# Kernel optimization log

Hardware: AMD Instinct MI355X
Metric: run time of the kernel (lower is better)

The kernel has to match this reference:

```python
import jax, jax.numpy as jnp
import numpy as np

DIM = 1024
H = 16
HD = 64

def setup_inputs() -> dict:
    key = jax.random.key(0)
    ks = jax.random.split(key, 5)
    x = jax.random.normal(ks[0], (2, 2048, DIM), dtype=jnp.float32)
    gamma = jnp.ones((DIM,), jnp.float32)
    beta = jnp.zeros((DIM,), jnp.float32)
    w_qkv = jax.random.normal(ks[1], (DIM, 3 * H * HD), dtype=jnp.float32) * (DIM ** -0.5)
    w_out = jax.random.normal(ks[2], (H * HD, DIM), dtype=jnp.float32) * ((H * HD) ** -0.5)
    b_out = jnp.zeros((DIM,), jnp.float32)
    return {"x": x, "gamma": gamma, "beta": beta, "w_qkv": w_qkv, "w_out": w_out, "b_out": b_out}

def reference(x, gamma, beta, w_qkv, w_out, b_out):
    # LayerNorm (pre-norm)
    mu = jnp.mean(x, axis=-1, keepdims=True)
    var = jnp.var(x, axis=-1, keepdims=True)
    xn = (x - mu) * jax.lax.rsqrt(var + 1e-5) * gamma + beta
    # QKV projection (no bias)
    qkv = xn @ w_qkv  # (b, n, 3*h*hd)
    q, k, v = jnp.split(qkv, 3, axis=-1)
    b, n, _ = x.shape
    split = lambda t: t.reshape(b, n, H, HD).transpose(0, 2, 1, 3)  # b h n d
    q, k, v = split(q), split(k), split(v)
    scale = HD ** -0.5
    scores = jnp.einsum('bhqd,bhkd->bhqk', q, k) * scale
    weights = jax.nn.softmax(scores, axis=-1)
    attn = jnp.einsum('bhqk,bhkd->bhqd', weights, v)  # b h n d
    attn = attn.transpose(0, 2, 1, 3).reshape(b, n, H * HD)
    # output projection (dropout is identity in eval)
    return attn @ w_out + b_out
```

## Files before the change

### kernel.cpp

```cpp
#include <hip/hip_runtime.h>
#include <hip/hip_bf16.h>


typedef _Float16 f16x8 __attribute__((ext_vector_type(8)));
typedef _Float16 f16x4 __attribute__((ext_vector_type(4)));
typedef float    f32x4 __attribute__((ext_vector_type(4)));

#define DIM   1024
#define NH    16
#define HD2   64
#define SEQ   2048
#define ROWS  4096
#define QKVN  3072

__device__ __forceinline__ void async_copy16(void* lds, const void* gsrc) {
    __builtin_amdgcn_global_load_lds(
        (const __attribute__((address_space(1))) unsigned int*)gsrc,
        (__attribute__((address_space(3))) unsigned int*)lds, 16, 0, 0);
}

__global__ __launch_bounds__(256) void prologue_kernel(
    const float* __restrict__ x, const float* __restrict__ gamma,
    const float* __restrict__ beta, _Float16* __restrict__ xn,
    const float* __restrict__ w_qkv, _Float16* __restrict__ wqkvT,
    const float* __restrict__ w_out, _Float16* __restrict__ woutT) {
    __shared__ float smem[32 * 33];
    const int bid = blockIdx.x;
    const int t = threadIdx.x;
    if (bid < ROWS) {
        const int row = bid;
        const float4 v = reinterpret_cast<const float4*>(x + (size_t)row * DIM)[t];
        float s1 = v.x + v.y + v.z + v.w;
        float s2 = v.x * v.x + v.y * v.y + v.z * v.z + v.w * v.w;
        for (int off = 32; off; off >>= 1) {
            s1 += __shfl_down(s1, off);
            s2 += __shfl_down(s2, off);
        }
        const int wv = t >> 6, lane = t & 63;
        if (lane == 0) { smem[wv * 2] = s1; smem[wv * 2 + 1] = s2; }
        __syncthreads();
        s1 = smem[0] + smem[2] + smem[4] + smem[6];
        s2 = smem[1] + smem[3] + smem[5] + smem[7];
        const float mu = s1 * (1.0f / DIM);
        const float var = s2 * (1.0f / DIM) - mu * mu;
        const float rstd = rsqrtf(var + 1e-5f);
        const float4 g = reinterpret_cast<const float4*>(gamma)[t];
        const float4 bb = reinterpret_cast<const float4*>(beta)[t];
        f16x4 o;
        o[0] = (_Float16)((v.x - mu) * rstd * g.x + bb.x);
        o[1] = (_Float16)((v.y - mu) * rstd * g.y + bb.y);
        o[2] = (_Float16)((v.z - mu) * rstd * g.z + bb.z);
        o[3] = (_Float16)((v.w - mu) * rstd * g.w + bb.w);
        reinterpret_cast<f16x4*>(xn + (size_t)row * DIM)[t] = o;
        return;
    }
    const float* in;
    _Float16* out;
    int C, bx, by;
    if (bid < ROWS + (QKVN / 32) * (DIM / 32)) {
        const int q = bid - ROWS;
        in = w_qkv; out = wqkvT; C = QKVN;
        bx = q % (QKVN / 32); by = q / (QKVN / 32);
    } else {
        const int q = bid - ROWS - (QKVN / 32) * (DIM / 32);
        in = w_out; out = woutT; C = DIM;
        bx = q % (DIM / 32); by = q / (DIM / 32);
    }
    const int R = DIM;
    const int c0 = bx * 32, r0 = by * 32;
    const int tx = t & 31, ty = t >> 5;
    float (*tile)[33] = reinterpret_cast<float(*)[33]>(smem);
#pragma unroll
    for (int i = 0; i < 4; i++)
        tile[ty + i * 8][tx] = in[(size_t)(r0 + ty + i * 8) * C + c0 + tx];
    __syncthreads();
#pragma unroll
    for (int i = 0; i < 4; i++)
        out[(size_t)(c0 + ty + i * 8) * R + r0 + tx] = (_Float16)tile[tx][ty + i * 8];
}

__global__ __launch_bounds__(256) void gemm_qkv_kernel(
    const _Float16* __restrict__ A, const _Float16* __restrict__ Bt,
    _Float16* __restrict__ qk, _Float16* __restrict__ vT, int K) {
    __shared__ _Float16 Al[2][128 * 32];
    __shared__ _Float16 Bl[2][128 * 32];
    const int t = threadIdx.x, wv = t >> 6, lane = t & 63;
    const int lg = lane >> 4, lr = lane & 15;
    const int wr = wv >> 1, wc = wv & 1;
    const int id = blockIdx.x;
    const int nid = (id & 7) * 96 + (id >> 3);
    const int bx = nid / 32, by = nid % 32;
    const int m0 = by * 128, n0 = bx * 128;

    f32x4 acc[4][4] = {};

    const int srow = t >> 2, sk = (t & 3) * 8;
    const _Float16* Ag0 = A + (size_t)(m0 + srow) * K + sk;
    const _Float16* Bg0 = Bt + (size_t)(n0 + srow) * K + sk;

    auto STAGE = [&](int buf, int k0) {
        _Float16* Alw = &Al[buf][wv * 512];
        _Float16* Blw = &Bl[buf][wv * 512];
        async_copy16(Alw,        Ag0 + k0);
        async_copy16(Alw + 2048, Ag0 + (size_t)64 * K + k0);
        async_copy16(Blw,        Bg0 + k0);
        async_copy16(Blw + 2048, Bg0 + (size_t)64 * K + k0);
    };

    STAGE(0, 0);
    asm volatile("s_waitcnt vmcnt(0)" ::: "memory");
    __builtin_amdgcn_s_barrier();
    int cur = 0;
    for (int k0 = 0; k0 < K; k0 += 32) {
        if (k0 + 32 < K) STAGE(cur ^ 1, k0 + 32);
        const _Float16* Ab = &Al[cur][0];
        const _Float16* Bb = &Bl[cur][0];
        f16x8 af[4], bfr[4];
#pragma unroll
        for (int m = 0; m < 4; m++)
            af[m] = *reinterpret_cast<const f16x8*>(&Ab[(wr * 64 + m * 16 + lr) * 32 + lg * 8]);
#pragma unroll
        for (int n = 0; n < 4; n++)
            bfr[n] = *reinterpret_cast<const f16x8*>(&Bb[(wc * 64 + n * 16 + lr) * 32 + lg * 8]);
#pragma unroll
        for (int m = 0; m < 4; m++)
#pragma unroll
            for (int n = 0; n < 4; n++)
                acc[m][n] = __builtin_amdgcn_mfma_f32_16x16x32_f16(af[m], bfr[n], acc[m][n], 0, 0, 0);
        asm volatile("s_waitcnt vmcnt(0)" ::: "memory");
        __builtin_amdgcn_s_barrier();
        cur ^= 1;
    }

    if (n0 < 2 * DIM) {
#pragma unroll
        for (int m = 0; m < 4; m++) {
            const int row = m0 + wr * 64 + m * 16 + lg * 4;
#pragma unroll
            for (int n = 0; n < 4; n++) {
                const int col = n0 + wc * 64 + n * 16 + lr;
#pragma unroll
                for (int jj = 0; jj < 4; jj++)
                    qk[(size_t)(row + jj) * 2048 + col] = (_Float16)acc[m][n][jj];
            }
        }
    } else {
#pragma unroll
        for (int m = 0; m < 4; m++) {
            const int row = m0 + wr * 64 + m * 16 + lg * 4;
            const int b = row >> 11, nn = row & 2047;
#pragma unroll
            for (int n = 0; n < 4; n++) {
                const int vcol = n0 + wc * 64 + n * 16 + lr - 2 * DIM;
                f16x4 pk;
#pragma unroll
                for (int jj = 0; jj < 4; jj++) pk[jj] = (_Float16)acc[m][n][jj];
                *reinterpret_cast<f16x4*>(&vT[(size_t)(b * 1024 + vcol) * SEQ + nn]) = pk;
            }
        }
    }
}

__global__ __launch_bounds__(256) void gemm_out_kernel(
    const _Float16* __restrict__ A, const _Float16* __restrict__ Bt,
    float* __restrict__ C, const float* __restrict__ bias, int N, int K) {
    __shared__ _Float16 Al[2][128 * 32];
    __shared__ _Float16 Bl[2][64 * 32];
    const int t = threadIdx.x, wv = t >> 6, lane = t & 63;
    const int lg = lane >> 4, lr = lane & 15;
    const int wr = wv >> 1, wc = wv & 1;
    const int id = blockIdx.x;
    const int nid = (id & 7) * 64 + (id >> 3);
    const int bx = nid / 32, by = nid % 32;
    const int m0 = by * 128, n0 = bx * 64;

    f32x4 acc[4][2] = {};

    const int srow = t >> 2, sk = (t & 3) * 8;
    const _Float16* Ag0 = A + (size_t)(m0 + srow) * K + sk;
    const _Float16* Bg0 = Bt + (size_t)(n0 + srow) * K + sk;

    auto STAGE = [&](int buf, int k0) {
        _Float16* Alw = &Al[buf][wv * 512];
        _Float16* Blw = &Bl[buf][wv * 512];
        async_copy16(Alw,        Ag0 + k0);
        async_copy16(Alw + 2048, Ag0 + (size_t)64 * K + k0);
        async_copy16(Blw,        Bg0 + k0);
    };

    STAGE(0, 0);
    asm volatile("s_waitcnt vmcnt(0)" ::: "memory");
    __builtin_amdgcn_s_barrier();
    int cur = 0;
    for (int k0 = 0; k0 < K; k0 += 32) {
        if (k0 + 32 < K) STAGE(cur ^ 1, k0 + 32);
        const _Float16* Ab = &Al[cur][0];
        const _Float16* Bb = &Bl[cur][0];
        f16x8 af[4], bfr[2];
#pragma unroll
        for (int m = 0; m < 4; m++)
            af[m] = *reinterpret_cast<const f16x8*>(&Ab[(wr * 64 + m * 16 + lr) * 32 + lg * 8]);
#pragma unroll
        for (int n = 0; n < 2; n++)
            bfr[n] = *reinterpret_cast<const f16x8*>(&Bb[(wc * 32 + n * 16 + lr) * 32 + lg * 8]);
#pragma unroll
        for (int m = 0; m < 4; m++)
#pragma unroll
            for (int n = 0; n < 2; n++)
                acc[m][n] = __builtin_amdgcn_mfma_f32_16x16x32_f16(af[m], bfr[n], acc[m][n], 0, 0, 0);
        asm volatile("s_waitcnt vmcnt(0)" ::: "memory");
        __builtin_amdgcn_s_barrier();
        cur ^= 1;
    }

#pragma unroll
    for (int m = 0; m < 4; m++) {
        const int row = m0 + wr * 64 + m * 16 + lg * 4;
#pragma unroll
        for (int n = 0; n < 2; n++) {
            const int col = n0 + wc * 32 + n * 16 + lr;
            const float bo = bias[col];
#pragma unroll
            for (int jj = 0; jj < 4; jj++)
                C[(size_t)(row + jj) * N + col] = acc[m][n][jj] + bo;
        }
    }
}

__global__ __launch_bounds__(256, 2) void attn_fa_kernel(
    const _Float16* __restrict__ qk, const _Float16* __restrict__ vT,
    _Float16* __restrict__ attn) {
    const int id = blockIdx.x;
    const int nid = (id & 7) * 64 + (id >> 3);
    const int bh = nid >> 4, b = bh >> 4, h = bh & 15;
    const int q0 = (nid & 15) * 128;
    const int t = threadIdx.x, wv = t >> 6, lane = t & 63;
    const int lg = lane >> 4, lr = lane & 15;

    __shared__ _Float16 Kl[2][64][76];
    __shared__ _Float16 Vt[2][64][76];

    const _Float16* qb = qk + (size_t)(b * SEQ + q0 + wv * 32 + lr) * 2048 + h * HD2;
    f16x8 qf[2][2];
    qf[0][0] = *reinterpret_cast<const f16x8*>(qb + lg * 8);
    qf[0][1] = *reinterpret_cast<const f16x8*>(qb + 32 + lg * 8);
    qf[1][0] = *reinterpret_cast<const f16x8*>(qb + (size_t)16 * 2048 + lg * 8);
    qf[1][1] = *reinterpret_cast<const f16x8*>(qb + (size_t)16 * 2048 + 32 + lg * 8);
#pragma unroll
    for (int qs = 0; qs < 2; qs++) {
        qf[qs][0] = qf[qs][0] * (_Float16)0.125f;
        qf[qs][1] = qf[qs][1] * (_Float16)0.125f;
    }

    f32x4 o[2][4] = {};
    float mrun[2] = {-INFINITY, -INFINITY}, lrun[2] = {0.f, 0.f};

    const int sr = t >> 3, sc = (t & 7) * 8;
    const _Float16* kbase = qk + (size_t)(b * SEQ + sr) * 2048 + DIM + h * HD2 + sc;
    const _Float16* vbase = vT + (size_t)(bh * HD2 + sr) * SEQ + sc;

    f16x8 rk0 = *reinterpret_cast<const f16x8*>(kbase);
    f16x8 rk1 = *reinterpret_cast<const f16x8*>(kbase + (size_t)32 * 2048);
    f16x8 rv0 = *reinterpret_cast<const f16x8*>(vbase);
    f16x8 rv1 = *reinterpret_cast<const f16x8*>(vbase + (size_t)32 * SEQ);
    *reinterpret_cast<f16x8*>(&Kl[0][sr][sc])      = rk0;
    *reinterpret_cast<f16x8*>(&Kl[0][sr + 32][sc]) = rk1;
    *reinterpret_cast<f16x8*>(&Vt[0][sr][sc])      = rv0;
    *reinterpret_cast<f16x8*>(&Vt[0][sr + 32][sc]) = rv1;
    rk0 = *reinterpret_cast<const f16x8*>(kbase + (size_t)64 * 2048);
    rk1 = *reinterpret_cast<const f16x8*>(kbase + (size_t)96 * 2048);
    rv0 = *reinterpret_cast<const f16x8*>(vbase + 64);
    rv1 = *reinterpret_cast<const f16x8*>(vbase + (size_t)32 * SEQ + 64);
    asm volatile("s_waitcnt lgkmcnt(0)" ::: "memory");
    __builtin_amdgcn_s_barrier();

    int p = 0;
    for (int kv0 = 0; kv0 < SEQ; kv0 += 64, p ^= 1) {
        if (kv0 + 64 < SEQ) {
            *reinterpret_cast<f16x8*>(&Kl[p ^ 1][sr][sc])      = rk0;
            *reinterpret_cast<f16x8*>(&Kl[p ^ 1][sr + 32][sc]) = rk1;
            *reinterpret_cast<f16x8*>(&Vt[p ^ 1][sr][sc])      = rv0;
            *reinterpret_cast<f16x8*>(&Vt[p ^ 1][sr + 32][sc]) = rv1;
            if (kv0 + 128 < SEQ) {
                const _Float16* kp = kbase + (size_t)(kv0 + 128) * 2048;
                const _Float16* vp = vbase + (kv0 + 128);
                rk0 = *reinterpret_cast<const f16x8*>(kp);
                rk1 = *reinterpret_cast<const f16x8*>(kp + (size_t)32 * 2048);
                rv0 = *reinterpret_cast<const f16x8*>(vp);
                rv1 = *reinterpret_cast<const f16x8*>(vp + (size_t)32 * SEQ);
            }
        }

        f32x4 s[2][4];
#pragma unroll
        for (int n = 0; n < 4; n++) {
            f16x8 kf0 = *reinterpret_cast<const f16x8*>(&Kl[p][n * 16 + lr][lg * 8]);
            f16x8 kf1 = *reinterpret_cast<const f16x8*>(&Kl[p][n * 16 + lr][32 + lg * 8]);
            __builtin_amdgcn_s_setprio(1);
#pragma unroll
            for (int qs = 0; qs < 2; qs++) {
                f32x4 z = {0.f, 0.f, 0.f, 0.f};
                z = __builtin_amdgcn_mfma_f32_16x16x32_f16(kf0, qf[qs][0], z, 0, 0, 0);
                z = __builtin_amdgcn_mfma_f32_16x16x32_f16(kf1, qf[qs][1], z, 0, 0, 0);
                s[qs][n] = z;
            }
            __builtin_amdgcn_s_setprio(0);
        }

        f16x8 pa[2][2];
#pragma unroll
        for (int qs = 0; qs < 2; qs++) {
            f32x4 m4a = s[qs][0], m4b = s[qs][2];
#pragma unroll
            for (int jj = 0; jj < 4; jj++) {
                m4a[jj] = fmaxf(m4a[jj], s[qs][1][jj]);
                m4b[jj] = fmaxf(m4b[jj], s[qs][3][jj]);
            }
            float m1 = fmaxf(fmaxf(fmaxf(m4a[0], m4b[0]), fmaxf(m4a[1], m4b[1])),
                             fmaxf(fmaxf(m4a[2], m4b[2]), fmaxf(m4a[3], m4b[3])));
            m1 = fmaxf(m1, __shfl_xor(m1, 16));
            m1 = fmaxf(m1, __shfl_xor(m1, 32));
            if (!__all(m1 - mrun[qs] <= 8.f)) {
                const float mnew = fmaxf(mrun[qs], m1);
                const float corr = __expf(mrun[qs] - mnew);
                mrun[qs] = mnew;
                lrun[qs] *= corr;
#pragma unroll
                for (int dn = 0; dn < 4; dn++) o[qs][dn] *= corr;
            }
#pragma unroll
            for (int n = 0; n < 4; n++)
#pragma unroll
                for (int jj = 0; jj < 4; jj++)
                    s[qs][n][jj] = __expf(s[qs][n][jj] - mrun[qs]);
            f32x4 a4 = s[qs][0] + s[qs][1];
            f32x4 b4 = s[qs][2] + s[qs][3];
            a4 = a4 + b4;
            float rsum = (a4[0] + a4[1]) + (a4[2] + a4[3]);
            rsum += __shfl_xor(rsum, 16);
            rsum += __shfl_xor(rsum, 32);
            lrun[qs] += rsum;
#pragma unroll
            for (int m = 0; m < 2; m++) {
                f16x8 pv;
#pragma unroll
                for (int jj = 0; jj < 4; jj++) {
                    pv[jj]     = (_Float16)s[qs][2 * m][jj];
                    pv[4 + jj] = (_Float16)s[qs][2 * m + 1][jj];
                }
                pa[qs][m] = pv;
            }
        }

#pragma unroll
        for (int dn = 0; dn < 4; dn++) {
            const _Float16* vr = &Vt[p][dn * 16 + lr][0];
            f16x4 va0 = *reinterpret_cast<const f16x4*>(vr + lg * 4);
            f16x4 va1 = *reinterpret_cast<const f16x4*>(vr + 16 + lg * 4);
            f16x4 vb0 = *reinterpret_cast<const f16x4*>(vr + 32 + lg * 4);
            f16x4 vb1 = *reinterpret_cast<const f16x4*>(vr + 48 + lg * 4);
            f16x8 vf0, vf1;
#pragma unroll
            for (int j = 0; j < 4; j++) {
                vf0[j] = va0[j]; vf0[4 + j] = va1[j];
                vf1[j] = vb0[j]; vf1[4 + j] = vb1[j];
            }
            __builtin_amdgcn_s_setprio(1);
#pragma unroll
            for (int qs = 0; qs < 2; qs++) {
                o[qs][dn] = __builtin_amdgcn_mfma_f32_16x16x32_f16(vf0, pa[qs][0], o[qs][dn], 0, 0, 0);
                o[qs][dn] = __builtin_amdgcn_mfma_f32_16x16x32_f16(vf1, pa[qs][1], o[qs][dn], 0, 0, 0);
            }
            __builtin_amdgcn_s_setprio(0);
        }
        asm volatile("s_waitcnt lgkmcnt(0)" ::: "memory");
        __builtin_amdgcn_s_barrier();
    }

#pragma unroll
    for (int qs = 0; qs < 2; qs++) {
        const float inv = 1.0f / lrun[qs];
        const size_t orow = (size_t)(b * SEQ + q0 + wv * 32 + qs * 16 + lr);
#pragma unroll
        for (int dn = 0; dn < 4; dn++) {
            f16x4 pk;
#pragma unroll
            for (int jj = 0; jj < 4; jj++) pk[jj] = (_Float16)(o[qs][dn][jj] * inv);
            *reinterpret_cast<f16x4*>(&attn[orow * DIM + h * HD2 + dn * 16 + lg * 4]) = pk;
        }
    }
}

extern "C" void kernel_launch(void* const* d_in, const int* in_sizes, int n_in,
                              void* d_out, int out_size, void* d_ws, size_t ws_size,
                              hipStream_t stream) {
    const float* x     = (const float*)d_in[0];
    const float* gamma = (const float*)d_in[1];
    const float* beta  = (const float*)d_in[2];
    const float* w_qkv = (const float*)d_in[3];
    const float* w_out = (const float*)d_in[4];
    const float* b_out = (const float*)d_in[5];
    float* out = (float*)d_out;

    _Float16* ws    = (_Float16*)d_ws;
    _Float16* xn    = ws;
    _Float16* wqkvT = xn + (size_t)ROWS * DIM;
    _Float16* woutT = wqkvT + (size_t)QKVN * DIM;
    _Float16* qk    = woutT + (size_t)DIM * DIM;
    _Float16* vT    = qk + (size_t)ROWS * 2048;
    _Float16* attnb = xn;

    const int pro_blocks = ROWS + (QKVN / 32) * (DIM / 32) + (DIM / 32) * (DIM / 32);
    prologue_kernel<<<pro_blocks, 256, 0, stream>>>(x, gamma, beta, xn, w_qkv, wqkvT, w_out, woutT);
    gemm_qkv_kernel<<<768, 256, 0, stream>>>(xn, wqkvT, qk, vT, DIM);
    attn_fa_kernel<<<512, 256, 0, stream>>>(qk, vT, attnb);
    gemm_out_kernel<<<512, 256, 0, stream>>>(attnb, woutT, out, b_out, DIM, DIM);
}
```

Baseline: 200.8 us.

## Software-pipeline attention loop: overlap previous tile's PV MFMAs with current softmax

Restructures the flash-attention main loop so the P·V matrix multiply for the previous KV tile is issued after the current tile's QK^T, with the V fragments read into registers ahead of time. The goal is to let the MFMA work of PV overlap the exp/max/sum softmax VALU work and the LDS reads instead of running them back to back. The cost is more live registers (V fragments and P kept across iterations), which could lower occupancy or cause spills.

Measured after the change: 197.2 us. About the same (-1.8%).

```diff
diff --git a/kernel.cpp b/kernel.cpp
--- a/kernel.cpp
+++ b/kernel.cpp
@@ -259,39 +259,28 @@
     const _Float16* kbase = qk + (size_t)(b * SEQ + sr) * 2048 + DIM + h * HD2 + sc;
     const _Float16* vbase = vT + (size_t)(bh * HD2 + sr) * SEQ + sc;
 
-    f16x8 rk0 = *reinterpret_cast<const f16x8*>(kbase);
-    f16x8 rk1 = *reinterpret_cast<const f16x8*>(kbase + (size_t)32 * 2048);
-    f16x8 rv0 = *reinterpret_cast<const f16x8*>(vbase);
-    f16x8 rv1 = *reinterpret_cast<const f16x8*>(vbase + (size_t)32 * SEQ);
-    *reinterpret_cast<f16x8*>(&Kl[0][sr][sc])      = rk0;
-    *reinterpret_cast<f16x8*>(&Kl[0][sr + 32][sc]) = rk1;
-    *reinterpret_cast<f16x8*>(&Vt[0][sr][sc])      = rv0;
-    *reinterpret_cast<f16x8*>(&Vt[0][sr + 32][sc]) = rv1;
-    rk0 = *reinterpret_cast<const f16x8*>(kbase + (size_t)64 * 2048);
-    rk1 = *reinterpret_cast<const f16x8*>(kbase + (size_t)96 * 2048);
-    rv0 = *reinterpret_cast<const f16x8*>(vbase + 64);
-    rv1 = *reinterpret_cast<const f16x8*>(vbase + (size_t)32 * SEQ + 64);
-    asm volatile("s_waitcnt lgkmcnt(0)" ::: "memory");
-    __builtin_amdgcn_s_barrier();
-
-    int p = 0;
-    for (int kv0 = 0; kv0 < SEQ; kv0 += 64, p ^= 1) {
-        if (kv0 + 64 < SEQ) {
-            *reinterpret_cast<f16x8*>(&Kl[p ^ 1][sr][sc])      = rk0;
-            *reinterpret_cast<f16x8*>(&Kl[p ^ 1][sr + 32][sc]) = rk1;
-            *reinterpret_cast<f16x8*>(&Vt[p ^ 1][sr][sc])      = rv0;
-            *reinterpret_cast<f16x8*>(&Vt[p ^ 1][sr + 32][sc]) = rv1;
-            if (kv0 + 128 < SEQ) {
-                const _Float16* kp = kbase + (size_t)(kv0 + 128) * 2048;
-                const _Float16* vp = vbase + (kv0 + 128);
-                rk0 = *reinterpret_cast<const f16x8*>(kp);
-                rk1 = *reinterpret_cast<const f16x8*>(kp + (size_t)32 * 2048);
-                rv0 = *reinterpret_cast<const f16x8*>(vp);
-                rv1 = *reinterpret_cast<const f16x8*>(vp + (size_t)32 * SEQ);
-            }
-        }
-
-        f32x4 s[2][4];
+    f16x8 rk0, rk1, rv0, rv1;
+
+    f32x4 s[2][4];
+    f16x8 vfr[4][2];
+    f16x8 pa[2][2];
+
+    auto STAGEW = [&](int pb, int kv_next) {
+        *reinterpret_cast<f16x8*>(&Kl[pb][sr][sc])      = rk0;
+        *reinterpret_cast<f16x8*>(&Kl[pb][sr + 32][sc]) = rk1;
+        *reinterpret_cast<f16x8*>(&Vt[pb][sr][sc])      = rv0;
+        *reinterpret_cast<f16x8*>(&Vt[pb][sr + 32][sc]) = rv1;
+        if (kv_next + 64 < SEQ) {
+            const _Float16* kp = kbase + (size_t)(kv_next + 64) * 2048;
+            const _Float16* vp = vbase + (kv_next + 64);
+            rk0 = *reinterpret_cast<const f16x8*>(kp);
+            rk1 = *reinterpret_cast<const f16x8*>(kp + (size_t)32 * 2048);
+            rv0 = *reinterpret_cast<const f16x8*>(vp);
+            rv1 = *reinterpret_cast<const f16x8*>(vp + (size_t)32 * SEQ);
+        }
+    };
+
+    auto QK = [&](int p) {
 #pragma unroll
         for (int n = 0; n < 4; n++) {
             f16x8 kf0 = *reinterpret_cast<const f16x8*>(&Kl[p][n * 16 + lr][lg * 8]);
@@ -306,8 +295,40 @@
             }
             __builtin_amdgcn_s_setprio(0);
         }
-
-        f16x8 pa[2][2];
+    };
+
+    auto READV = [&](int p) {
+#pragma unroll
+        for (int dn = 0; dn < 4; dn++) {
+            const _Float16* vr = &Vt[p][dn * 16 + lr][0];
+            f16x4 va0 = *reinterpret_cast<const f16x4*>(vr + lg * 4);
+            f16x4 va1 = *reinterpret_cast<const f16x4*>(vr + 16 + lg * 4);
+            f16x4 vb0 = *reinterpret_cast<const f16x4*>(vr + 32 + lg * 4);
+            f16x4 vb1 = *reinterpret_cast<const f16x4*>(vr + 48 + lg * 4);
+            f16x8 vf0, vf1;
+#pragma unroll
+            for (int j = 0; j < 4; j++) {
+                vf0[j] = va0[j]; vf0[4 + j] = va1[j];
+                vf1[j] = vb0[j]; vf1[4 + j] = vb1[j];
+            }
+            vfr[dn][0] = vf0; vfr[dn][1] = vf1;
+        }
+    };
+
+    auto PV = [&]() {
+#pragma unroll
+        for (int dn = 0; dn < 4; dn++) {
+            __builtin_amdgcn_s_setprio(1);
+#pragma unroll
+            for (int qs = 0; qs < 2; qs++) {
+                o[qs][dn] = __builtin_amdgcn_mfma_f32_16x16x32_f16(vfr[dn][0], pa[qs][0], o[qs][dn], 0, 0, 0);
+                o[qs][dn] = __builtin_amdgcn_mfma_f32_16x16x32_f16(vfr[dn][1], pa[qs][1], o[qs][dn], 0, 0, 0);
+            }
+            __builtin_amdgcn_s_setprio(0);
+        }
+    };
+
+    auto SOFTMAX = [&]() {
 #pragma unroll
         for (int qs = 0; qs < 2; qs++) {
             f32x4 m4a = s[qs][0], m4b = s[qs][2];
@@ -333,9 +354,7 @@
 #pragma unroll
                 for (int jj = 0; jj < 4; jj++)
                     s[qs][n][jj] = __expf(s[qs][n][jj] - mrun[qs]);
-            f32x4 a4 = s[qs][0] + s[qs][1];
-            f32x4 b4 = s[qs][2] + s[qs][3];
-            a4 = a4 + b4;
+            f32x4 a4 = (s[qs][0] + s[qs][1]) + (s[qs][2] + s[qs][3]);
             float rsum = (a4[0] + a4[1]) + (a4[2] + a4[3]);
             rsum += __shfl_xor(rsum, 16);
             rsum += __shfl_xor(rsum, 32);
@@ -351,31 +370,45 @@
                 pa[qs][m] = pv;
             }
         }
-
-#pragma unroll
-        for (int dn = 0; dn < 4; dn++) {
-            const _Float16* vr = &Vt[p][dn * 16 + lr][0];
-            f16x4 va0 = *reinterpret_cast<const f16x4*>(vr + lg * 4);
-            f16x4 va1 = *reinterpret_cast<const f16x4*>(vr + 16 + lg * 4);
-            f16x4 vb0 = *reinterpret_cast<const f16x4*>(vr + 32 + lg * 4);
-            f16x4 vb1 = *reinterpret_cast<const f16x4*>(vr + 48 + lg * 4);
-            f16x8 vf0, vf1;
-#pragma unroll
-            for (int j = 0; j < 4; j++) {
-                vf0[j] = va0[j]; vf0[4 + j] = va1[j];
-                vf1[j] = vb0[j]; vf1[4 + j] = vb1[j];
-            }
-            __builtin_amdgcn_s_setprio(1);
-#pragma unroll
-            for (int qs = 0; qs < 2; qs++) {
-                o[qs][dn] = __builtin_amdgcn_mfma_f32_16x16x32_f16(vf0, pa[qs][0], o[qs][dn], 0, 0, 0);
-                o[qs][dn] = __builtin_amdgcn_mfma_f32_16x16x32_f16(vf1, pa[qs][1], o[qs][dn], 0, 0, 0);
-            }
-            __builtin_amdgcn_s_setprio(0);
-        }
+    };
+
+    rk0 = *reinterpret_cast<const f16x8*>(kbase);
+    rk1 = *reinterpret_cast<const f16x8*>(kbase + (size_t)32 * 2048);
+    rv0 = *reinterpret_cast<const f16x8*>(vbase);
+    rv1 = *reinterpret_cast<const f16x8*>(vbase + (size_t)32 * SEQ);
+    *reinterpret_cast<f16x8*>(&Kl[0][sr][sc])      = rk0;
+    *reinterpret_cast<f16x8*>(&Kl[0][sr + 32][sc]) = rk1;
+    *reinterpret_cast<f16x8*>(&Vt[0][sr][sc])      = rv0;
+    *reinterpret_cast<f16x8*>(&Vt[0][sr + 32][sc]) = rv1;
+    {
+        const _Float16* kp = kbase + (size_t)64 * 2048;
+        const _Float16* vp = vbase + 64;
+        rk0 = *reinterpret_cast<const f16x8*>(kp);
+        rk1 = *reinterpret_cast<const f16x8*>(kp + (size_t)32 * 2048);
+        rv0 = *reinterpret_cast<const f16x8*>(vp);
+        rv1 = *reinterpret_cast<const f16x8*>(vp + (size_t)32 * SEQ);
+    }
+    asm volatile("s_waitcnt lgkmcnt(0)" ::: "memory");
+    __builtin_amdgcn_s_barrier();
+
+    STAGEW(1, 64);
+    QK(0);
+    READV(0);
+    SOFTMAX();
+    asm volatile("s_waitcnt lgkmcnt(0)" ::: "memory");
+    __builtin_amdgcn_s_barrier();
+
+    int p = 1;
+    for (int kv0 = 64; kv0 < SEQ; kv0 += 64, p ^= 1) {
+        if (kv0 + 64 < SEQ) STAGEW(p ^ 1, kv0 + 64);
+        QK(p);
+        PV();
+        READV(p);
+        SOFTMAX();
         asm volatile("s_waitcnt lgkmcnt(0)" ::: "memory");
         __builtin_amdgcn_s_barrier();
     }
+    PV();
 
 #pragma unroll
     for (int qs = 0; qs < 2; qs++) {
```
